# Kernel optimization log

Measured on AMD Instinct MI355X. Metric: run time of the kernel, lower is better.

Reference implementation:

```python
import jax, jax.numpy as jnp
import numpy as np


def _project(img_feat, x, y):
    """Bilinear gather. img_feat: [C,S,S]; x,y: [N] float coords. Returns [N,C]."""
    s = img_feat.shape[-1]
    x = jnp.clip(x, 0.0, s - 1)
    y = jnp.clip(y, 0.0, s - 1)
    x1 = jnp.floor(x).astype(jnp.int32)
    x2 = jnp.ceil(x).astype(jnp.int32)
    y1 = jnp.floor(y).astype(jnp.int32)
    y2 = jnp.ceil(y).astype(jnp.int32)
    # gathers: [C,N] -> transpose to [N,C]
    Q11 = img_feat[:, x1, y1].T
    Q12 = img_feat[:, x1, y2].T
    Q21 = img_feat[:, x2, y1].T
    Q22 = img_feat[:, x2, y2].T
    x1f, x2f = x1.astype(x.dtype), x2.astype(x.dtype)
    y1f, y2f = y1.astype(y.dtype), y2.astype(y.dtype)
    out = ((x2f - x) * (y2f - y))[:, None] * Q11 \
        + ((x - x1f) * (y2f - y))[:, None] * Q21 \
        + ((x2f - x) * (y - y1f))[:, None] * Q12 \
        + ((x - x1f) * (y - y1f))[:, None] * Q22
    return out


def _forward_solo(coord, f1, f2, f3, f4):
    # coord: [N,3]; f_i: [C_i, S_i, S_i]
    X, Y, Z = coord[:, 0], coord[:, 1], coord[:, 2]
    h = jnp.clip(250.0 * (-Y) / (-Z) + 112.0, 0.0, 223.0)
    w = jnp.clip(250.0 * X / (-Z) + 112.0, 0.0, 223.0)
    out1 = _project(f1, h / (224.0 / 56), w / (224.0 / 56))
    out2 = _project(f2, h / (224.0 / 28), w / (224.0 / 28))
    out3 = _project(f3, h / (224.0 / 14), w / (224.0 / 14))
    out4 = _project(f4, h / (224.0 / 7), w / (224.0 / 7))
    return jnp.concatenate([coord, out1, out2, out3, out4], axis=1)  # [N, 3+64+128+256+512]


def setup_inputs() -> dict:
    key = jax.random.key(0)
    k0, k1, k2, k3, k4, k5 = jax.random.split(key, 6)
    B, N = 4, 50000
    xy = jax.random.normal(k0, (B, N, 2), dtype=jnp.float32) * 0.5
    # Z strictly negative (camera looks down -Z); keeps -Z >= 1 so projection is finite
    z = -(1.0 + jax.random.uniform(k5, (B, N, 1), dtype=jnp.float32))
    inputs = jnp.concatenate([xy, z], axis=-1)  # [B,N,3]
    f1 = jax.random.normal(k1, (B, 64, 56, 56), dtype=jnp.float32)
    f2 = jax.random.normal(k2, (B, 128, 28, 28), dtype=jnp.float32)
    f3 = jax.random.normal(k3, (B, 256, 14, 14), dtype=jnp.float32)
    f4 = jax.random.normal(k4, (B, 512, 7, 7), dtype=jnp.float32)
    return {"inputs": inputs, "f1": f1, "f2": f2, "f3": f3, "f4": f4}


def reference(inputs, f1, f2, f3, f4):
    # Faithful to original: forward_solo is always called with inputs[0]
    coord0 = inputs[0]
    solo = lambda a, b, c, d: _forward_solo(coord0, a, b, c, d)
    return jax.vmap(solo)(f1, f2, f3, f4)  # [B, N, 963]
```

## Files before the change

### kernel.cpp

```cpp
#include <hip/hip_runtime.h>
#include <cstdint>
#include <cstddef>

#define ROW 963

__device__ __forceinline__ float bf2f(unsigned short u) {
    return __uint_as_float(((unsigned int)u) << 16);
}
__device__ __forceinline__ unsigned short f2bf(float v) {
    unsigned int u = __float_as_uint(v);
    u += 0x7FFFu + ((u >> 16) & 1u);
    return (unsigned short)(u >> 16);
}

__global__ __launch_bounds__(256) void trans_all_k(
    const float* __restrict__ f1, const float* __restrict__ f2,
    const float* __restrict__ f3, const float* __restrict__ f4,
    unsigned short* __restrict__ o1, unsigned short* __restrict__ o2,
    unsigned short* __restrict__ o3, unsigned short* __restrict__ o4) {
    int r = blockIdx.x * 256 + threadIdx.x;
    int b = blockIdx.y;
    const float* src; unsigned short* dst; int C, SS, rr, c, sp;
    if (r < 200704)      { src = f1; dst = o1; C = 64;  SS = 3136; rr = r;
                           c = rr / 3136; sp = rr - c * 3136; }
    else if (r < 301056) { src = f2; dst = o2; C = 128; SS = 784;  rr = r - 200704;
                           c = rr / 784;  sp = rr - c * 784; }
    else if (r < 351232) { src = f3; dst = o3; C = 256; SS = 196;  rr = r - 301056;
                           c = rr / 196;  sp = rr - c * 196; }
    else if (r < 376320) { src = f4; dst = o4; C = 512; SS = 49;   rr = r - 351232;
                           c = rr / 49;   sp = rr - c * 49; }
    else return;
    float v = src[(size_t)b * C * SS + rr];
    dst[((size_t)b * SS + sp) * C + c] = f2bf(v);
}

__global__ __launch_bounds__(256) void proj_bf16_k(
    const float* __restrict__ coord,
    const unsigned short* __restrict__ t1, const unsigned short* __restrict__ t2,
    const unsigned short* __restrict__ t3, const unsigned short* __restrict__ t4,
    float* __restrict__ out, int N) {
    int n = blockIdx.x;
    int b = blockIdx.y;
    int t = threadIdx.x;

    __shared__ float row[ROW + 1];

    float X = coord[3 * n + 0];
    float Y = coord[3 * n + 1];
    float Z = coord[3 * n + 2];
    float h = fminf(fmaxf((250.0f * -Y) / (-Z) + 112.0f, 0.0f), 223.0f);
    float w = fminf(fmaxf((250.0f * X) / (-Z) + 112.0f, 0.0f), 223.0f);

    if (t < 3) row[t] = coord[3 * n + t];

    if (t < 240) {
        const unsigned short* T; int S, C, cs;
        if (t < 16)       { T = t1; S = 56; C = 64;  cs = 0; }
        else if (t < 48)  { T = t2; S = 28; C = 128; cs = 16; }
        else if (t < 112) { T = t3; S = 14; C = 256; cs = 48; }
        else              { T = t4; S = 7;  C = 512; cs = 112; }
        int cc = (t - cs) * 4;

        float scale = (float)S * (1.0f / 224.0f);
        float sm1 = (float)(S - 1);
        float x = fminf(fmaxf(h * scale, 0.0f), sm1);
        float y = fminf(fmaxf(w * scale, 0.0f), sm1);
        float x1f = floorf(x), x2f = ceilf(x);
        float y1f = floorf(y), y2f = ceilf(y);
        int x1 = (int)x1f, x2 = (int)x2f;
        int y1 = (int)y1f, y2 = (int)y2f;

        const unsigned short* base = T + (size_t)b * (S * S) * C + cc;
        const ushort4* p11 = (const ushort4*)(base + (size_t)(x1 * S + y1) * C);
        const ushort4* p12 = (const ushort4*)(base + (size_t)(x1 * S + y2) * C);
        const ushort4* p21 = (const ushort4*)(base + (size_t)(x2 * S + y1) * C);
        const ushort4* p22 = (const ushort4*)(base + (size_t)(x2 * S + y2) * C);
        ushort4 q11 = *p11, q12 = *p12, q21 = *p21, q22 = *p22;

        float dx1 = x - x1f, dx2 = x2f - x;
        float dy1 = y - y1f, dy2 = y2f - y;
        float w11 = dx2 * dy2, w21 = dx1 * dy2, w12 = dx2 * dy1, w22 = dx1 * dy1;

        float v0 = w11 * bf2f(q11.x) + w21 * bf2f(q21.x) + w12 * bf2f(q12.x) + w22 * bf2f(q22.x);
        float v1 = w11 * bf2f(q11.y) + w21 * bf2f(q21.y) + w12 * bf2f(q12.y) + w22 * bf2f(q22.y);
        float v2 = w11 * bf2f(q11.z) + w21 * bf2f(q21.z) + w12 * bf2f(q12.z) + w22 * bf2f(q22.z);
        float v3 = w11 * bf2f(q11.w) + w21 * bf2f(q21.w) + w12 * bf2f(q12.w) + w22 * bf2f(q22.w);

        int o = 3 + 4 * t;
        row[o + 0] = v0; row[o + 1] = v1; row[o + 2] = v2; row[o + 3] = v3;
    }
    __syncthreads();

    size_t orow = ((size_t)b * N + n) * ROW;
    #pragma unroll
    for (int i = t; i < ROW; i += 256) out[orow + i] = row[i];
}

__global__ __launch_bounds__(256) void proj_nchw_k(
    const float* __restrict__ coord,
    const float* __restrict__ f1, const float* __restrict__ f2,
    const float* __restrict__ f3, const float* __restrict__ f4,
    float* __restrict__ out, int N) {
    int n = blockIdx.x, b = blockIdx.y;
    float X = coord[3 * n + 0], Y = coord[3 * n + 1], Z = coord[3 * n + 2];
    float h = fminf(fmaxf((250.0f * -Y) / (-Z) + 112.0f, 0.0f), 223.0f);
    float w = fminf(fmaxf((250.0f * X) / (-Z) + 112.0f, 0.0f), 223.0f);
    size_t orow = ((size_t)b * N + n) * ROW;
    if (threadIdx.x < 3) out[orow + threadIdx.x] = coord[3 * n + threadIdx.x];
    for (int c = threadIdx.x; c < 960; c += 256) {
        const float* T; int S, C, cc;
        if (c < 64)       { T = f1; S = 56; C = 64;  cc = c; }
        else if (c < 192) { T = f2; S = 28; C = 128; cc = c - 64; }
        else if (c < 448) { T = f3; S = 14; C = 256; cc = c - 192; }
        else              { T = f4; S = 7;  C = 512; cc = c - 448; }
        float scale = (float)S * (1.0f / 224.0f);
        float sm1 = (float)(S - 1);
        float x = fminf(fmaxf(h * scale, 0.0f), sm1);
        float y = fminf(fmaxf(w * scale, 0.0f), sm1);
        float x1f = floorf(x), x2f = ceilf(x);
        float y1f = floorf(y), y2f = ceilf(y);
        int x1 = (int)x1f, x2 = (int)x2f, y1 = (int)y1f, y2 = (int)y2f;
        const float* base = T + ((size_t)b * C + cc) * (size_t)(S * S);
        float Q11 = base[x1 * S + y1], Q12 = base[x1 * S + y2];
        float Q21 = base[x2 * S + y1], Q22 = base[x2 * S + y2];
        float dx1 = x - x1f, dx2 = x2f - x, dy1 = y - y1f, dy2 = y2f - y;
        out[orow + 3 + c] = (dx2 * dy2) * Q11 + (dx1 * dy2) * Q21 +
                            (dx2 * dy1) * Q12 + (dx1 * dy1) * Q22;
    }
}

extern "C" void kernel_launch(void* const* d_in, const int* in_sizes, int n_in,
                              void* d_out, int out_size, void* d_ws, size_t ws_size,
                              hipStream_t stream) {
    const float* inputs = (const float*)d_in[0];
    const float* f1 = (const float*)d_in[1];
    const float* f2 = (const float*)d_in[2];
    const float* f3 = (const float*)d_in[3];
    const float* f4 = (const float*)d_in[4];
    float* out = (float*)d_out;

    int B = in_sizes[1] / (64 * 56 * 56);
    int N = in_sizes[0] / (B * 3);

    size_t n1 = (size_t)B * 200704;
    size_t n2 = (size_t)B * 100352;
    size_t n3 = (size_t)B * 50176;
    size_t n4 = (size_t)B * 25088;
    size_t need = (n1 + n2 + n3 + n4) * sizeof(unsigned short);

    dim3 blk(256);
    if (ws_size >= need) {
        unsigned short* o1 = (unsigned short*)d_ws;
        unsigned short* o2 = o1 + n1;
        unsigned short* o3 = o2 + n2;
        unsigned short* o4 = o3 + n3;
        trans_all_k<<<dim3((376320 + 255) / 256, B), blk, 0, stream>>>(
            f1, f2, f3, f4, o1, o2, o3, o4);
        proj_bf16_k<<<dim3(N, B), blk, 0, stream>>>(inputs, o1, o2, o3, o4, out, N);
    } else {
        proj_nchw_k<<<dim3(N, B), blk, 0, stream>>>(inputs, f1, f2, f3, f4, out, N);
    }
}
```

Measured before the change: 858.2 us.

## Use persistent grid-stride projection with batch loop and direct global stores

The projection kernel becomes persistent: a fixed grid of at most 2048 blocks strides over points. Each block computes the projection coordinates and bilinear weights once per point and loops over the batch, writing results straight to global memory with no shared-memory staging or barrier. The transpose kernel now walks the output in linear order and uses shift/mask indexing instead of division, so its bf16 stores are coalesced and its fp32 reads are strided. The risks are that the direct stores to the 963-float rows are misaligned scalar writes, and that fewer blocks may hide memory latency less well.

```diff
diff --git a/kernel.cpp b/kernel.cpp
--- a/kernel.cpp
+++ b/kernel.cpp
@@ -20,80 +20,76 @@
     unsigned short* __restrict__ o3, unsigned short* __restrict__ o4) {
     int r = blockIdx.x * 256 + threadIdx.x;
     int b = blockIdx.y;
-    const float* src; unsigned short* dst; int C, SS, rr, c, sp;
-    if (r < 200704)      { src = f1; dst = o1; C = 64;  SS = 3136; rr = r;
-                           c = rr / 3136; sp = rr - c * 3136; }
-    else if (r < 301056) { src = f2; dst = o2; C = 128; SS = 784;  rr = r - 200704;
-                           c = rr / 784;  sp = rr - c * 784; }
-    else if (r < 351232) { src = f3; dst = o3; C = 256; SS = 196;  rr = r - 301056;
-                           c = rr / 196;  sp = rr - c * 196; }
-    else if (r < 376320) { src = f4; dst = o4; C = 512; SS = 49;   rr = r - 351232;
-                           c = rr / 49;   sp = rr - c * 49; }
-    else return;
-    float v = src[(size_t)b * C * SS + rr];
-    dst[((size_t)b * SS + sp) * C + c] = f2bf(v);
+    const float* src; unsigned short* dst; int SS, rr, lc;
+    if (r < 200704)      { src = f1; dst = o1; SS = 3136; rr = r;          lc = 6; }
+    else if (r < 301056) { src = f2; dst = o2; SS = 784;  rr = r - 200704; lc = 7; }
+    else if (r < 351232) { src = f3; dst = o3; SS = 196;  rr = r - 301056; lc = 8; }
+    else                 { src = f4; dst = o4; SS = 49;   rr = r - 351232; lc = 9; }
+    int C  = 1 << lc;
+    int c  = rr & (C - 1);
+    int sp = rr >> lc;
+    float v = src[(size_t)b * ((size_t)C * SS) + (size_t)c * SS + sp];
+    dst[(size_t)b * ((size_t)SS * C) + rr] = f2bf(v);
 }
 
 __global__ __launch_bounds__(256) void proj_bf16_k(
     const float* __restrict__ coord,
     const unsigned short* __restrict__ t1, const unsigned short* __restrict__ t2,
     const unsigned short* __restrict__ t3, const unsigned short* __restrict__ t4,
-    float* __restrict__ out, int N) {
-    int n = blockIdx.x;
-    int b = blockIdx.y;
+    float* __restrict__ out, int N, int B) {
     int t = threadIdx.x;
 
-    __shared__ float row[ROW + 1];
+    const unsigned short* T; int S, C, cs;
+    if (t < 16)       { T = t1; S = 56; C = 64;  cs = 0; }
+    else if (t < 48)  { T = t2; S = 28; C = 128; cs = 16; }
+    else if (t < 112) { T = t3; S = 14; C = 256; cs = 48; }
+    else              { T = t4; S = 7;  C = 512; cs = 112; }
+    int cc = (t - cs) * 4;
+    float scale = (float)S * (1.0f / 224.0f);
+    float sm1 = (float)(S - 1);
+    size_t lvl = (size_t)(S * S) * C;
+    bool active = (t < 240);
 
-    float X = coord[3 * n + 0];
-    float Y = coord[3 * n + 1];
-    float Z = coord[3 * n + 2];
-    float h = fminf(fmaxf((250.0f * -Y) / (-Z) + 112.0f, 0.0f), 223.0f);
-    float w = fminf(fmaxf((250.0f * X) / (-Z) + 112.0f, 0.0f), 223.0f);
-
-    if (t < 3) row[t] = coord[3 * n + t];
-
-    if (t < 240) {
-        const unsigned short* T; int S, C, cs;
-        if (t < 16)       { T = t1; S = 56; C = 64;  cs = 0; }
-        else if (t < 48)  { T = t2; S = 28; C = 128; cs = 16; }
-        else if (t < 112) { T = t3; S = 14; C = 256; cs = 48; }
-        else              { T = t4; S = 7;  C = 512; cs = 112; }
-        int cc = (t - cs) * 4;
-
-        float scale = (float)S * (1.0f / 224.0f);
-        float sm1 = (float)(S - 1);
+    for (int n = blockIdx.x; n < N; n += gridDim.x) {
+        float X = coord[3 * n + 0];
+        float Y = coord[3 * n + 1];
+        float Z = coord[3 * n + 2];
+        float h = fminf(fmaxf((250.0f * -Y) / (-Z) + 112.0f, 0.0f), 223.0f);
+        float w = fminf(fmaxf((250.0f * X) / (-Z) + 112.0f, 0.0f), 223.0f);
         float x = fminf(fmaxf(h * scale, 0.0f), sm1);
         float y = fminf(fmaxf(w * scale, 0.0f), sm1);
         float x1f = floorf(x), x2f = ceilf(x);
         float y1f = floorf(y), y2f = ceilf(y);
         int x1 = (int)x1f, x2 = (int)x2f;
         int y1 = (int)y1f, y2 = (int)y2f;
-
-        const unsigned short* base = T + (size_t)b * (S * S) * C + cc;
-        const ushort4* p11 = (const ushort4*)(base + (size_t)(x1 * S + y1) * C);
-        const ushort4* p12 = (const ushort4*)(base + (size_t)(x1 * S + y2) * C);
-        const ushort4* p21 = (const ushort4*)(base + (size_t)(x2 * S + y1) * C);
-        const ushort4* p22 = (const ushort4*)(base + (size_t)(x2 * S + y2) * C);
-        ushort4 q11 = *p11, q12 = *p12, q21 = *p21, q22 = *p22;
-
         float dx1 = x - x1f, dx2 = x2f - x;
         float dy1 = y - y1f, dy2 = y2f - y;
         float w11 = dx2 * dy2, w21 = dx1 * dy2, w12 = dx2 * dy1, w22 = dx1 * dy1;
+        int i11 = (x1 * S + y1) * C + cc;
+        int i12 = (x1 * S + y2) * C + cc;
+        int i21 = (x2 * S + y1) * C + cc;
+        int i22 = (x2 * S + y2) * C + cc;
 
-        float v0 = w11 * bf2f(q11.x) + w21 * bf2f(q21.x) + w12 * bf2f(q12.x) + w22 * bf2f(q22.x);
-        float v1 = w11 * bf2f(q11.y) + w21 * bf2f(q21.y) + w12 * bf2f(q12.y) + w22 * bf2f(q22.y);
-        float v2 = w11 * bf2f(q11.z) + w21 * bf2f(q21.z) + w12 * bf2f(q12.z) + w22 * bf2f(q22.z);
-        float v3 = w11 * bf2f(q11.w) + w21 * bf2f(q21.w) + w12 * bf2f(q12.w) + w22 * bf2f(q22.w);
-
-        int o = 3 + 4 * t;
-        row[o + 0] = v0; row[o + 1] = v1; row[o + 2] = v2; row[o + 3] = v3;
+        for (int b = 0; b < B; ++b) {
+            size_t orow = ((size_t)b * N + n) * ROW;
+            if (active) {
+                const unsigned short* base = T + (size_t)b * lvl;
+                ushort4 q11 = *(const ushort4*)(base + i11);
+                ushort4 q12 = *(const ushort4*)(base + i12);
+                ushort4 q21 = *(const ushort4*)(base + i21);
+                ushort4 q22 = *(const ushort4*)(base + i22);
+                float v0 = w11 * bf2f(q11.x) + w21 * bf2f(q21.x) + w12 * bf2f(q12.x) + w22 * bf2f(q22.x);
+                float v1 = w11 * bf2f(q11.y) + w21 * bf2f(q21.y) + w12 * bf2f(q12.y) + w22 * bf2f(q22.y);
+                float v2 = w11 * bf2f(q11.z) + w21 * bf2f(q21.z) + w12 * bf2f(q12.z) + w22 * bf2f(q22.z);
+                float v3 = w11 * bf2f(q11.w) + w21 * bf2f(q21.w) + w12 * bf2f(q12.w) + w22 * bf2f(q22.w);
+                size_t o = orow + 3 + 4 * (size_t)t;
+                out[o + 0] = v0; out[o + 1] = v1;
+                out[o + 2] = v2; out[o + 3] = v3;
+            } else if (t < 243) {
+                out[orow + (t - 240)] = (t == 240) ? X : (t == 241) ? Y : Z;
+            }
+        }
     }
-    __syncthreads();
-
-    size_t orow = ((size_t)b * N + n) * ROW;
-    #pragma unroll
-    for (int i = t; i < ROW; i += 256) out[orow + i] = row[i];
 }
 
 __global__ __launch_bounds__(256) void proj_nchw_k(
@@ -154,9 +150,10 @@
         unsigned short* o2 = o1 + n1;
         unsigned short* o3 = o2 + n2;
         unsigned short* o4 = o3 + n3;
-        trans_all_k<<<dim3((376320 + 255) / 256, B), blk, 0, stream>>>(
+        trans_all_k<<<dim3(376320 / 256, B), blk, 0, stream>>>(
             f1, f2, f3, f4, o1, o2, o3, o4);
-        proj_bf16_k<<<dim3(N, B), blk, 0, stream>>>(inputs, o1, o2, o3, o4, out, N);
+        int nblk = N < 2048 ? N : 2048;
+        proj_bf16_k<<<dim3(nblk), blk, 0, stream>>>(inputs, o1, o2, o3, o4, out, N, B);
     } else {
         proj_nchw_k<<<dim3(N, B), blk, 0, stream>>>(inputs, f1, f2, f3, f4, out, N);
     }
```

Measured after the change: 824.1 us. 1.04x faster.
